# Kernel optimization log

Hardware: AMD Instinct MI355X
Metric: run time of the kernel (lower is better)

The kernel has to match this reference:

```python
import jax, jax.numpy as jnp
import numpy as np

DIM_S, DIM_A, DIM_C, H, T = 64, 8, 16, 256, 262144
LOG_STD_MIN, LOG_STD_MAX = -5.0, 2.0


def _linear_init(k, fin, fout):
    k1, k2 = jax.random.split(k)
    lim = 1.0 / np.sqrt(fin)
    W = jax.random.uniform(k1, (fin, fout), minval=-lim, maxval=lim, dtype=jnp.float32)
    b = jax.random.uniform(k2, (fout,), minval=-lim, maxval=lim, dtype=jnp.float32)
    return W, b


def setup_inputs() -> dict:
    key = jax.random.key(0)
    ks = jax.random.split(key, 8)
    pW1, pb1 = _linear_init(ks[0], DIM_S, H)
    pW2, pb2 = _linear_init(ks[1], H, H)
    pW3, pb3 = _linear_init(ks[2], H, DIM_C * DIM_A)
    oW1, ob1 = _linear_init(ks[3], DIM_S, H)
    oW2, ob2 = _linear_init(ks[4], H, H)
    oW3, ob3 = _linear_init(ks[5], H, (DIM_C + 1) * DIM_C)
    a_log_std = jnp.zeros((1, DIM_A), jnp.float32)
    s_array = jax.random.normal(ks[6], (T, DIM_S), jnp.float32)
    a_array = jax.random.normal(ks[7], (T, DIM_A), jnp.float32)
    return dict(s_array=s_array, a_array=a_array,
                pW1=pW1, pb1=pb1, pW2=pW2, pb2=pb2, pW3=pW3, pb3=pb3,
                oW1=oW1, ob1=ob1, oW2=oW2, ob2=ob2, oW3=oW3, ob3=ob3,
                a_log_std=a_log_std)


def _mlp(x, W1, b1, W2, b2, W3, b3):
    h = jax.nn.relu(x @ W1 + b1)
    h = jax.nn.relu(h @ W2 + b2)
    return h @ W3 + b3


def reference(s_array, a_array, pW1, pb1, pW2, pb2, pW3, pb3,
              oW1, ob1, oW2, ob2, oW3, ob3, a_log_std):
    Tn = s_array.shape[0]
    # --- log_prob_action with ct=None: per-option Gaussian log-density ---
    mean = _mlp(s_array, pW1, pb1, pW2, pb2, pW3, pb3).reshape(Tn, DIM_C, DIM_A)
    mean = jnp.clip(mean, -10.0, 10.0)
    logstd = LOG_STD_MIN + 0.5 * (LOG_STD_MAX - LOG_STD_MIN) * (jnp.tanh(a_log_std) + 1.0)  # (1, A), shared across options
    std = jnp.exp(logstd)
    at = a_array[:, None, :]                                   # (T, 1, A)
    lp = -0.5 * ((at - mean) / std) ** 2 - logstd - 0.5 * jnp.log(2.0 * jnp.pi)
    log_pis = lp.sum(-1)                                       # (T, C)
    # --- log_trans: normalized option-transition logits ---
    logits = _mlp(s_array, oW1, ob1, oW2, ob2, oW3, ob3).reshape(Tn, DIM_C + 1, DIM_C)
    log_trs_full = jax.nn.log_softmax(logits, axis=-1)
    log_tr0 = log_trs_full[0, -1]                              # (C,) initial dist from c_{-1}=dim_c
    log_trs = log_trs_full[1:, :-1]                            # (T-1, C, C)
    # --- forward recursion (alpha) via scan ---
    a0 = log_tr0 + log_pis[0]
    def fwd_step(carry, x):
        ltr, lpi = x
        a = jax.nn.logsumexp(carry[:, None] + ltr, axis=0) + lpi
        return a, a
    _, alphas = jax.lax.scan(fwd_step, a0, (log_trs, log_pis[1:]))
    log_alpha = jnp.concatenate([a0[None], alphas], axis=0)    # (T, C)
    # --- backward recursion (beta) via reverse scan ---
    bT = jnp.zeros((DIM_C,), jnp.float32)
    def bwd_step(carry, x):
        ltr, lpi = x
        b = jax.nn.logsumexp((carry + lpi)[None, :] + ltr, axis=-1)
        return b, b
    _, betas = jax.lax.scan(bwd_step, bT, (log_trs, log_pis[1:]), reverse=True)
    log_beta = jnp.concatenate([betas, bT[None]], axis=0)      # (T, C)
    entropy = -(log_trs * jnp.exp(log_trs)).sum(-1)            # (T-1, C)
    return (log_alpha, log_beta, log_trs, log_pis, entropy)
```

## Files before the change

### kernel.cpp

```cpp
#include <hip/hip_runtime.h>
#include <hip/hip_bf16.h>
#include <math.h>

#define T_N   262144
#define NSTEP (T_N - 1)
#define CS    256
#define NC    1024
#define NG    32

#define OFF_A   ((size_t)0)
#define OFF_B   ((size_t)4194304)
#define OFF_LTR ((size_t)8388608)
#define OFF_LPI ((size_t)75497216)
#define OFF_ENT ((size_t)79691520)

#define WS_TR0  ((size_t)0)
#define WS_M    ((size_t)64)
#define WS_LP   (WS_M  + (size_t)NC*256)
#define WS_LS   (WS_LP + (size_t)NC*256)
#define WS_GT   (WS_LS + (size_t)NC*256)
#define WS_GP   (WS_GT + (size_t)NG*256)
#define WS_GSU  (WS_GP + (size_t)NG*256)
#define WS_PREF (WS_GSU + (size_t)NG*256)
#define WS_SUF  (WS_PREF + (size_t)NC*256)
#define WS_WP   (WS_SUF  + (size_t)NC*256)

#define O_pW1h 0
#define O_pW1l 16384
#define O_pW2h 32768
#define O_pW2l 98304
#define O_pW3h 163840
#define O_pW3l 196608
#define O_oW1h 229376
#define O_oW1l 245760
#define O_oW2h 262144
#define O_oW2l 327680
#define O_oW3h 393216
#define O_oW3l 462848

#define NEGINF (-1e30f)

typedef unsigned short ushort_t;
typedef short s8v __attribute__((ext_vector_type(8)));
typedef float f4v __attribute__((ext_vector_type(4)));

__device__ __forceinline__ ushort_t f2bf_rn(float f) {
  __hip_bfloat16 h = __float2bfloat16(f);
  union { __hip_bfloat16 b; ushort_t u; } cv; cv.b = h; return cv.u;
}
__device__ __forceinline__ float us2f(ushort_t u) {
  return __uint_as_float(((unsigned)u) << 16);
}
__device__ __forceinline__ void split_bf(float x, ushort_t& h, ushort_t& lo) {
  unsigned u = __float_as_uint(x);
  h = (ushort_t)(u >> 16);
  lo = f2bf_rn(x - __uint_as_float(u & 0xffff0000u));
}

__global__ void k_pack(const float* __restrict__ W, int KN, int NT, int N,
                       ushort_t* __restrict__ dh, ushort_t* __restrict__ dl)
{
  int idx = blockIdx.x * 256 + threadIdx.x;
  if (idx >= KN) return;
  int j  = idx & 7;
  int l  = (idx >> 3) & 63;
  int t2 = idx >> 9;
  int nt = t2 % NT;
  int ks = t2 / NT;
  int k = ks * 32 + (l >> 4) * 8 + j;
  int n = nt * 16 + (l & 15);
  float x = W[(size_t)k * N + n];
  unsigned u = __float_as_uint(x);
  dh[idx] = (ushort_t)(u >> 16);
  dl[idx] = f2bf_rn(x - __uint_as_float(u & 0xffff0000u));
}


#define LDX 72
#define LDH 264

template<int KS, int NTC>
__device__ __forceinline__ void run_layer(const ushort_t* Ah, const ushort_t* Al, int lda,
    const ushort_t* __restrict__ Bh, const ushort_t* __restrict__ Bl, int ntt, int nt0,
    const float* __restrict__ bias, int lane, f4v (&acc)[2][NTC])
{
#pragma unroll
  for (int mt = 0; mt < 2; mt++)
#pragma unroll
    for (int nt = 0; nt < NTC; nt++) {
      float b = bias[(nt0 + nt) * 16 + (lane & 15)];
      acc[mt][nt] = (f4v){b, b, b, b};
    }
  for (int ks = 0; ks < KS; ks++) {
    s8v ah[2], al[2];
#pragma unroll
    for (int mt = 0; mt < 2; mt++) {
      const ushort_t* p = Ah + (size_t)(mt * 16 + (lane & 15)) * lda + ks * 32 + (lane >> 4) * 8;
      ah[mt] = *(const s8v*)p;
      const ushort_t* q = Al + (size_t)(mt * 16 + (lane & 15)) * lda + ks * 32 + (lane >> 4) * 8;
      al[mt] = *(const s8v*)q;
    }
#pragma unroll
    for (int nt = 0; nt < NTC; nt++) {
      size_t bo = ((size_t)(ks * ntt + nt0 + nt) * 64 + lane) * 8;
      s8v bh = *(const s8v*)(Bh + bo);
      s8v bl = *(const s8v*)(Bl + bo);
#pragma unroll
      for (int mt = 0; mt < 2; mt++) {
        acc[mt][nt] = __builtin_amdgcn_mfma_f32_16x16x32_bf16(ah[mt], bh, acc[mt][nt], 0, 0, 0);
        acc[mt][nt] = __builtin_amdgcn_mfma_f32_16x16x32_bf16(al[mt], bh, acc[mt][nt], 0, 0, 0);
        acc[mt][nt] = __builtin_amdgcn_mfma_f32_16x16x32_bf16(ah[mt], bl, acc[mt][nt], 0, 0, 0);
      }
    }
  }
}

__device__ __forceinline__ void store_act(f4v (&acc)[2][4], int nt0, int lane,
                                          ushort_t* Hh, ushort_t* Hl)
{
#pragma unroll
  for (int mt = 0; mt < 2; mt++)
#pragma unroll
    for (int nt = 0; nt < 4; nt++)
#pragma unroll
      for (int r = 0; r < 4; r++) {
        float v = fmaxf(acc[mt][nt][r], 0.f);
        ushort_t h, lo; split_bf(v, h, lo);
        int row = mt * 16 + (lane >> 4) * 4 + r;
        int n = (nt0 + nt) * 16 + (lane & 15);
        Hh[row * LDH + n] = h;
        Hl[row * LDH + n] = lo;
      }
}

__launch_bounds__(256, 3)
__global__ void k_mlp2(const float* __restrict__ s_array, const float* __restrict__ a_array,
                       const float* __restrict__ pb1, const float* __restrict__ pb2,
                       const float* __restrict__ pb3, const float* __restrict__ ob1,
                       const float* __restrict__ ob2, const float* __restrict__ ob3,
                       const float* __restrict__ oW3, const float* __restrict__ als,
                       const ushort_t* __restrict__ wp, float* out, float* ws)
{
  __shared__ ushort_t Xh[32 * LDX], Xl[32 * LDX];
  __shared__ ushort_t Hh[32 * LDH], Hl[32 * LDH];
  __shared__ float tr0s[16];
  const int tid = threadIdx.x;
  const int lane = tid & 63;
  const int w = tid >> 6;
  const size_t row0 = (size_t)blockIdx.x * 32;

  {
    const float4* src = (const float4*)(s_array + row0 * 64);
    for (int f = tid; f < 512; f += 256) {
      float4 v = src[f];
      int r = f >> 4, c = (f & 15) * 4;
      ushort_t h0, l0, h1, l1, h2, l2, h3, l3;
      split_bf(v.x, h0, l0); split_bf(v.y, h1, l1);
      split_bf(v.z, h2, l2); split_bf(v.w, h3, l3);
      ushort4 hh = make_ushort4(h0, h1, h2, h3);
      ushort4 ll = make_ushort4(l0, l1, l2, l3);
      *(ushort4*)&Xh[r * LDX + c] = hh;
      *(ushort4*)&Xl[r * LDX + c] = ll;
    }
  }
  __syncthreads();

  f4v acc[2][4];

  run_layer<2, 4>(Xh, Xl, LDX, wp + O_oW1h, wp + O_oW1l, 16, w * 4, ob1, lane, acc);
  store_act(acc, w * 4, lane, Hh, Hl);
  __syncthreads();
  run_layer<8, 4>(Hh, Hl, LDH, wp + O_oW2h, wp + O_oW2l, 16, w * 4, ob2, lane, acc);
  __syncthreads();
  store_act(acc, w * 4, lane, Hh, Hl);
  __syncthreads();
  run_layer<8, 4>(Hh, Hl, LDH, wp + O_oW3h, wp + O_oW3l, 17, w * 4, ob3, lane, acc);

#pragma unroll
  for (int mt = 0; mt < 2; mt++)
#pragma unroll
    for (int nt = 0; nt < 4; nt++) {
      int g = w * 4 + nt;
      int col = lane & 15;
#pragma unroll
      for (int r = 0; r < 4; r++) {
        size_t t = row0 + mt * 16 + (lane >> 4) * 4 + r;
        float x = acc[mt][nt][r];
        float m = x;
        m = fmaxf(m, __shfl_xor(m, 1, 64));
        m = fmaxf(m, __shfl_xor(m, 2, 64));
        m = fmaxf(m, __shfl_xor(m, 4, 64));
        m = fmaxf(m, __shfl_xor(m, 8, 64));
        float s = __expf(x - m);
        s += __shfl_xor(s, 1, 64);
        s += __shfl_xor(s, 2, 64);
        s += __shfl_xor(s, 4, 64);
        s += __shfl_xor(s, 8, 64);
        float L = m + __logf(s);
        float v = x - L;
        float e = -v * __expf(v);
        e += __shfl_xor(e, 1, 64);
        e += __shfl_xor(e, 2, 64);
        e += __shfl_xor(e, 4, 64);
        e += __shfl_xor(e, 8, 64);
        if (t >= 1) {
          out[OFF_LTR + (t - 1) * 256 + (size_t)g * 16 + col] = v;
          if (col == 0) out[OFF_ENT + (t - 1) * 16 + g] = e;
        }
      }
    }

  if (blockIdx.x == 0 && tid < 16) {
    float a = ob3[256 + tid];
    for (int k2 = 0; k2 < 256; k2++) {
      float hv = us2f(Hh[k2]) + us2f(Hl[k2]);
      a = fmaf(hv, oW3[(size_t)k2 * 272 + 256 + tid], a);
    }
    tr0s[tid] = a;
  }
  __syncthreads();
  if (blockIdx.x == 0 && tid == 0) {
    float m = NEGINF;
    for (int j = 0; j < 16; j++) m = fmaxf(m, tr0s[j]);
    float s = 0.f;
    for (int j = 0; j < 16; j++) s += __expf(tr0s[j] - m);
    float L = m + __logf(s);
    for (int j = 0; j < 16; j++) ws[WS_TR0 + j] = tr0s[j] - L;
  }

  run_layer<2, 4>(Xh, Xl, LDX, wp + O_pW1h, wp + O_pW1l, 16, w * 4, pb1, lane, acc);
  store_act(acc, w * 4, lane, Hh, Hl);
  __syncthreads();
  run_layer<8, 4>(Hh, Hl, LDH, wp + O_pW2h, wp + O_pW2l, 16, w * 4, pb2, lane, acc);
  __syncthreads();
  store_act(acc, w * 4, lane, Hh, Hl);
  __syncthreads();
  f4v pacc[2][2];
  run_layer<8, 2>(Hh, Hl, LDH, wp + O_pW3h, wp + O_pW3l, 8, w * 2, pb3, lane, pacc);

  float istd[8];
  float Kc = -8.0f * 0.91893853320467274f;
#pragma unroll
  for (int a = 0; a < 8; a++) {
    float l = -5.0f + 3.5f * (tanhf(als[a]) + 1.0f);
    istd[a] = __expf(-l);
    Kc -= l;
  }
  int aIdx = lane & 7;
#pragma unroll
  for (int mt = 0; mt < 2; mt++)
#pragma unroll
    for (int nt = 0; nt < 2; nt++) {
      int col = (w * 2 + nt) * 16 + (lane & 15);
      int c = col >> 3;
#pragma unroll
      for (int r = 0; r < 4; r++) {
        size_t t = row0 + mt * 16 + (lane >> 4) * 4 + r;
        float mean = fminf(10.f, fmaxf(-10.f, pacc[mt][nt][r]));
        float av = a_array[t * 8 + aIdx];
        float z = (av - mean) * istd[aIdx];
        float q = z * z;
        q += __shfl_xor(q, 1, 64);
        q += __shfl_xor(q, 2, 64);
        q += __shfl_xor(q, 4, 64);
        if ((lane & 7) == 0) out[OFF_LPI + t * 16 + c] = -0.5f * q + Kc;
      }
    }
}


#define LDA 20

__launch_bounds__(256, 4)
__global__ void k_compose(const float* __restrict__ out, float* __restrict__ ws)
{
  __shared__ float AsT[2][16 * LDA] __attribute__((aligned(16)));
  __shared__ float Mb[2][16 * 16] __attribute__((aligned(16)));
  __shared__ float Lsb[2][16];
  const int tid = threadIdx.x;
  const int i = tid >> 4, k = tid & 15;
  const int c = blockIdx.x;
  long long e0 = (long long)c * CS;
  long long e1 = e0 + CS; if (e1 > NSTEP) e1 = NSTEP;

  float a1, l1;
  {
    float a0 = out[OFF_LTR + (size_t)e0 * 256 + tid];
    AsT[0][k * LDA + i] = a0;
    if (tid < 16) Lsb[0][tid] = out[OFF_LPI + (size_t)(e0 + 1) * 16 + tid];
    Mb[0][tid] = (i == k) ? 0.f : NEGINF;
    a1 = out[OFF_LTR + (size_t)(e0 + 1) * 256 + tid];
    l1 = (tid < 16) ? out[OFF_LPI + (size_t)(e0 + 2) * 16 + tid] : 0.f;
  }
  __syncthreads();

  int cur = 0;
  float last = NEGINF;
  for (long long e = e0; e < e1; e++) {
    float a2 = out[OFF_LTR + (size_t)(e + 2) * 256 + tid];
    float l2 = (tid < 16) ? out[OFF_LPI + (size_t)(e + 3) * 16 + tid] : 0.f;

    float v[16];
    {
      const float4* M4 = (const float4*)&Mb[cur][i * 16];
      const float4* A4 = (const float4*)&AsT[cur][k * LDA];
#pragma unroll
      for (int t = 0; t < 4; t++) {
        float4 a = M4[t], b = A4[t];
        v[4 * t + 0] = a.x + b.x; v[4 * t + 1] = a.y + b.y;
        v[4 * t + 2] = a.z + b.z; v[4 * t + 3] = a.w + b.w;
      }
    }
    float m = NEGINF;
#pragma unroll
    for (int j = 0; j < 16; j++) m = fmaxf(m, v[j]);
    float s = 0.f;
#pragma unroll
    for (int j = 0; j < 16; j++) s += __expf(v[j] - m);
    last = m + __logf(s) + Lsb[cur][k];

    AsT[cur ^ 1][k * LDA + i] = a1;
    if (tid < 16) Lsb[cur ^ 1][tid] = l1;
    Mb[cur ^ 1][tid] = last;
    __syncthreads();
    a1 = a2; l1 = l2;
    cur ^= 1;
  }
  ws[WS_M + (size_t)c * 256 + tid] = last;
}


__launch_bounds__(256, 4)
__global__ void k_scan_mats(const float* __restrict__ src, float* __restrict__ preDst,
                            float* __restrict__ sufDst, float* __restrict__ totDst)
{
  __shared__ float Cur[16 * 17];
  const int tid = threadIdx.x, i = tid >> 4, k = tid & 15;
  const int g = blockIdx.x;
  const float* S = src + (size_t)g * 32 * 256;
  const float id = (i == k) ? 0.f : NEGINF;

  float rv[16], rn[16];
  Cur[i * 17 + k] = id;
#pragma unroll
  for (int j = 0; j < 16; j++) rv[j] = S[j * 16 + k];
  __syncthreads();
  for (int r = 0; r < 32; r++) {
    preDst[((size_t)g * 32 + r) * 256 + tid] = Cur[i * 17 + k];
    int rp = (r + 1 < 32) ? r + 1 : 31;
#pragma unroll
    for (int j = 0; j < 16; j++) rn[j] = S[(size_t)rp * 256 + j * 16 + k];
    float v[16]; float m = NEGINF;
#pragma unroll
    for (int j = 0; j < 16; j++) { v[j] = Cur[i * 17 + j] + rv[j]; m = fmaxf(m, v[j]); }
    float s = 0.f;
#pragma unroll
    for (int j = 0; j < 16; j++) s += __expf(v[j] - m);
    float res = m + __logf(s);
    __syncthreads();
    Cur[i * 17 + k] = res;
    __syncthreads();
#pragma unroll
    for (int j = 0; j < 16; j++) rv[j] = rn[j];
  }
  if (totDst) totDst[(size_t)g * 256 + tid] = Cur[i * 17 + k];
  __syncthreads();
  Cur[i * 17 + k] = id;
#pragma unroll
  for (int j = 0; j < 16; j++) rv[j] = S[(size_t)31 * 256 + i * 16 + j];
  __syncthreads();
  for (int r = 31; r >= 0; r--) {
    sufDst[((size_t)g * 32 + r) * 256 + tid] = Cur[i * 17 + k];
    int rp = (r > 0) ? r - 1 : 0;
#pragma unroll
    for (int j = 0; j < 16; j++) rn[j] = S[(size_t)rp * 256 + i * 16 + j];
    float v[16]; float m = NEGINF;
#pragma unroll
    for (int j = 0; j < 16; j++) { v[j] = rv[j] + Cur[j * 17 + k]; m = fmaxf(m, v[j]); }
    float s = 0.f;
#pragma unroll
    for (int j = 0; j < 16; j++) s += __expf(v[j] - m);
    float res = m + __logf(s);
    __syncthreads();
    Cur[i * 17 + k] = res;
    __syncthreads();
#pragma unroll
    for (int j = 0; j < 16; j++) rv[j] = rn[j];
  }
}


__launch_bounds__(256, 4)
__global__ void k_combine(float* ws)
{
  const int tid = threadIdx.x, i = tid >> 4, k = tid & 15;
  const int c = blockIdx.x, g = c >> 5;
  {
    const float* GP = ws + WS_GP + (size_t)g * 256;
    const float* LP = ws + WS_LP + (size_t)c * 256;
    float v[16]; float m = NEGINF;
#pragma unroll
    for (int j = 0; j < 16; j++) { v[j] = GP[i * 16 + j] + LP[j * 16 + k]; m = fmaxf(m, v[j]); }
    float s = 0.f;
#pragma unroll
    for (int j = 0; j < 16; j++) s += __expf(v[j] - m);
    ws[WS_PREF + (size_t)c * 256 + tid] = m + __logf(s);
  }
  {
    const float* LSu = ws + WS_LS + (size_t)c * 256;
    const float* GSu = ws + WS_GSU + (size_t)g * 256;
    float v[16]; float m = NEGINF;
#pragma unroll
    for (int j = 0; j < 16; j++) { v[j] = LSu[i * 16 + j] + GSu[j * 16 + k]; m = fmaxf(m, v[j]); }
    float s = 0.f;
#pragma unroll
    for (int j = 0; j < 16; j++) s += __expf(v[j] - m);
    ws[WS_SUF + (size_t)c * 256 + tid] = m + __logf(s);
  }
}


__device__ __forceinline__ void lse_combine(float& m, float& s, int mask)
{
  float m2 = __shfl_xor(m, mask, 64);
  float s2 = __shfl_xor(s, mask, 64);
  float M_ = fmaxf(m, m2);
  s = s * __expf(m - M_) + s2 * __expf(m2 - M_);
  m = M_;
}

__launch_bounds__(128, 4)
__global__ void k_replay(const float* __restrict__ ws, float* out)
{
  const int c = blockIdx.x;
  long long e0 = (long long)c * CS;
  long long e1 = e0 + CS; if (e1 > NSTEP) e1 = NSTEP;
  const int lane = threadIdx.x & 63;
  const int wv = threadIdx.x >> 6;
  const int x = lane & 15;
  const int q = lane >> 4;

  if (wv == 0) {
    if (c == 0 && lane < 16)
      out[OFF_A + lane] = ws[WS_TR0 + lane] + out[OFF_LPI + lane];
    const float* P = ws + WS_PREF + (size_t)c * 256;
    float v4[4]; float m = NEGINF;
#pragma unroll
    for (int t2 = 0; t2 < 4; t2++) {
      int i2 = 4 * q + t2;
      float a0i = ws[WS_TR0 + i2] + out[OFF_LPI + i2];
      float vv = a0i + P[i2 * 16 + x];
      v4[t2] = vv; m = fmaxf(m, vv);
    }
    float s = 0.f;
#pragma unroll
    for (int t2 = 0; t2 < 4; t2++) s += __expf(v4[t2] - m);
    lse_combine(m, s, 16); lse_combine(m, s, 32);
    float cv = m + __logf(s);
    float vq[4];
#pragma unroll
    for (int t2 = 0; t2 < 4; t2++) vq[t2] = __shfl(cv, q * 4 + t2, 64);

    float ta0[4], ta1[4], la0, la1;
#pragma unroll
    for (int t2 = 0; t2 < 4; t2++)
      ta0[t2] = out[OFF_LTR + (size_t)e0 * 256 + (size_t)(4 * q + t2) * 16 + x];
    la0 = out[OFF_LPI + (size_t)(e0 + 1) * 16 + x];
#pragma unroll
    for (int t2 = 0; t2 < 4; t2++)
      ta1[t2] = out[OFF_LTR + (size_t)(e0 + 1) * 256 + (size_t)(4 * q + t2) * 16 + x];
    la1 = out[OFF_LPI + (size_t)(e0 + 2) * 16 + x];

    for (long long e = e0; e < e1; e++) {
      float tn[4], ln;
#pragma unroll
      for (int t2 = 0; t2 < 4; t2++)
        tn[t2] = out[OFF_LTR + (size_t)(e + 2) * 256 + (size_t)(4 * q + t2) * 16 + x];
      ln = out[OFF_LPI + (size_t)(e + 3) * 16 + x];

      long long t = e + 1;
      float w4[4]; float m2 = NEGINF;
#pragma unroll
      for (int t2 = 0; t2 < 4; t2++) {
        float vvv = vq[t2] + ta0[t2];
        w4[t2] = vvv; m2 = fmaxf(m2, vvv);
      }
      float s2 = 0.f;
#pragma unroll
      for (int t2 = 0; t2 < 4; t2++) s2 += __expf(w4[t2] - m2);
      lse_combine(m2, s2, 16); lse_combine(m2, s2, 32);
      float nv = m2 + __logf(s2) + la0;
      if (lane < 16) out[OFF_A + (size_t)t * 16 + x] = nv;
#pragma unroll
      for (int t2 = 0; t2 < 4; t2++) vq[t2] = __shfl(nv, q * 4 + t2, 64);
#pragma unroll
      for (int t2 = 0; t2 < 4; t2++) { ta0[t2] = ta1[t2]; ta1[t2] = tn[t2]; }
      la0 = la1; la1 = ln;
    }
  } else {
    if (c == NC - 1 && lane < 16) out[OFF_B + (size_t)(T_N - 1) * 16 + lane] = 0.f;
    const float* Sf = ws + WS_SUF + (size_t)c * 256;
    float v4[4]; float m = NEGINF;
#pragma unroll
    for (int t2 = 0; t2 < 4; t2++) {
      float vv = Sf[x * 16 + 4 * q + t2];
      v4[t2] = vv; m = fmaxf(m, vv);
    }
    float s = 0.f;
#pragma unroll
    for (int t2 = 0; t2 < 4; t2++) s += __expf(v4[t2] - m);
    lse_combine(m, s, 16); lse_combine(m, s, 32);
    float u = m + __logf(s);
    float uq[4];
#pragma unroll
    for (int t2 = 0; t2 < 4; t2++) uq[t2] = __shfl(u, q * 4 + t2, 64);

    float tb0[4], tb1[4], lb0[4], lb1[4];
    {
      long long eA = e1 - 1, eB = e1 - 2;
      float4 f = *(const float4*)&out[(long long)OFF_LTR + eA * 256 + x * 16 + 4 * q];
      tb0[0] = f.x; tb0[1] = f.y; tb0[2] = f.z; tb0[3] = f.w;
      float4 g2 = *(const float4*)&out[(long long)OFF_LPI + (eA + 1) * 16 + 4 * q];
      lb0[0] = g2.x; lb0[1] = g2.y; lb0[2] = g2.z; lb0[3] = g2.w;
      float4 f2 = *(const float4*)&out[(long long)OFF_LTR + eB * 256 + x * 16 + 4 * q];
      tb1[0] = f2.x; tb1[1] = f2.y; tb1[2] = f2.z; tb1[3] = f2.w;
      float4 g3 = *(const float4*)&out[(long long)OFF_LPI + (eB + 1) * 16 + 4 * q];
      lb1[0] = g3.x; lb1[1] = g3.y; lb1[2] = g3.z; lb1[3] = g3.w;
    }

    for (long long e = e1 - 1; e >= e0; e--) {
      float tn[4], ln[4];
      {
        long long ep = e - 2;
        float4 f = *(const float4*)&out[(long long)OFF_LTR + ep * 256 + x * 16 + 4 * q];
        tn[0] = f.x; tn[1] = f.y; tn[2] = f.z; tn[3] = f.w;
        float4 g2 = *(const float4*)&out[(long long)OFF_LPI + (ep + 1) * 16 + 4 * q];
        ln[0] = g2.x; ln[1] = g2.y; ln[2] = g2.z; ln[3] = g2.w;
      }
      float w4[4]; float m2 = NEGINF;
#pragma unroll
      for (int t2 = 0; t2 < 4; t2++) {
        float vvv = tb0[t2] + lb0[t2] + uq[t2];
        w4[t2] = vvv; m2 = fmaxf(m2, vvv);
      }
      float s2 = 0.f;
#pragma unroll
      for (int t2 = 0; t2 < 4; t2++) s2 += __expf(w4[t2] - m2);
      lse_combine(m2, s2, 16); lse_combine(m2, s2, 32);
      float b = m2 + __logf(s2);
      if (lane < 16) out[OFF_B + (size_t)e * 16 + x] = b;
#pragma unroll
      for (int t2 = 0; t2 < 4; t2++) uq[t2] = __shfl(b, q * 4 + t2, 64);
#pragma unroll
      for (int t2 = 0; t2 < 4; t2++) {
        tb0[t2] = tb1[t2]; tb1[t2] = tn[t2];
        lb0[t2] = lb1[t2]; lb1[t2] = ln[t2];
      }
    }
  }
}


extern "C" void kernel_launch(void* const* d_in, const int* in_sizes, int n_in,
                              void* d_out, int out_size, void* d_ws, size_t ws_size,
                              hipStream_t stream)
{
  const float* s_array = (const float*)d_in[0];
  const float* a_array = (const float*)d_in[1];
  const float* pW1 = (const float*)d_in[2];
  const float* pb1 = (const float*)d_in[3];
  const float* pW2 = (const float*)d_in[4];
  const float* pb2 = (const float*)d_in[5];
  const float* pW3 = (const float*)d_in[6];
  const float* pb3 = (const float*)d_in[7];
  const float* oW1 = (const float*)d_in[8];
  const float* ob1 = (const float*)d_in[9];
  const float* oW2 = (const float*)d_in[10];
  const float* ob2 = (const float*)d_in[11];
  const float* oW3 = (const float*)d_in[12];
  const float* ob3 = (const float*)d_in[13];
  const float* als = (const float*)d_in[14];
  float* out = (float*)d_out;
  float* ws  = (float*)d_ws;
  ushort_t* wp = (ushort_t*)(ws + WS_WP);

  hipLaunchKernelGGL(k_pack, dim3(64),  dim3(256), 0, stream, pW1, 16384, 16, 256, wp + O_pW1h, wp + O_pW1l);
  hipLaunchKernelGGL(k_pack, dim3(256), dim3(256), 0, stream, pW2, 65536, 16, 256, wp + O_pW2h, wp + O_pW2l);
  hipLaunchKernelGGL(k_pack, dim3(128), dim3(256), 0, stream, pW3, 32768,  8, 128, wp + O_pW3h, wp + O_pW3l);
  hipLaunchKernelGGL(k_pack, dim3(64),  dim3(256), 0, stream, oW1, 16384, 16, 256, wp + O_oW1h, wp + O_oW1l);
  hipLaunchKernelGGL(k_pack, dim3(256), dim3(256), 0, stream, oW2, 65536, 16, 256, wp + O_oW2h, wp + O_oW2l);
  hipLaunchKernelGGL(k_pack, dim3(272), dim3(256), 0, stream, oW3, 69632, 17, 272, wp + O_oW3h, wp + O_oW3l);

  hipLaunchKernelGGL(k_mlp2, dim3(T_N / 32), dim3(256), 0, stream,
                     s_array, a_array, pb1, pb2, pb3, ob1, ob2, ob3, oW3, als,
                     (const ushort_t*)wp, out, ws);
  hipLaunchKernelGGL(k_compose, dim3(NC), dim3(256), 0, stream, out, ws);
  hipLaunchKernelGGL(k_scan_mats, dim3(NG), dim3(256), 0, stream,
                     ws + WS_M, ws + WS_LP, ws + WS_LS, ws + WS_GT);
  hipLaunchKernelGGL(k_scan_mats, dim3(1), dim3(256), 0, stream,
                     ws + WS_GT, ws + WS_GP, ws + WS_GSU, (float*)nullptr);
  hipLaunchKernelGGL(k_combine, dim3(NC), dim3(256), 0, stream, ws);
  hipLaunchKernelGGL(k_replay, dim3(NC), dim3(128), 0, stream, ws, out);
}
```

Measured before the change: 1.546 ms.

## Use wave-per-chunk shuffle-based log-semiring composition with finer chunking

Rewrites the chunk composition and hierarchical scan kernels so that one wavefront, rather than a whole block, handles each chunk. Each lane computes four outputs and the new row is broadcast with shuffles, which replaces the block-wide barrier on every step. The scan runs its forward and backward directions in separate waves, and the log-sum-exp uses a tree reduction. It also adds a finer chunking configuration (4096 chunks of 64 steps) that is selected when the workspace is large enough. The trade-off is more intermediate matrices to write, plus a fallback path to the old chunk sizes when the workspace is smaller.

```diff
diff --git a/kernel.cpp b/kernel.cpp
--- a/kernel.cpp
+++ b/kernel.cpp
@@ -4,9 +4,6 @@
 
 #define T_N   262144
 #define NSTEP (T_N - 1)
-#define CS    256
-#define NC    1024
-#define NG    32
 
 #define OFF_A   ((size_t)0)
 #define OFF_B   ((size_t)4194304)
@@ -15,15 +12,6 @@
 #define OFF_ENT ((size_t)79691520)
 
 #define WS_TR0  ((size_t)0)
-#define WS_M    ((size_t)64)
-#define WS_LP   (WS_M  + (size_t)NC*256)
-#define WS_LS   (WS_LP + (size_t)NC*256)
-#define WS_GT   (WS_LS + (size_t)NC*256)
-#define WS_GP   (WS_GT + (size_t)NG*256)
-#define WS_GSU  (WS_GP + (size_t)NG*256)
-#define WS_PREF (WS_GSU + (size_t)NG*256)
-#define WS_SUF  (WS_PREF + (size_t)NC*256)
-#define WS_WP   (WS_SUF  + (size_t)NC*256)
 
 #define O_pW1h 0
 #define O_pW1l 16384
@@ -43,6 +31,23 @@
 typedef unsigned short ushort_t;
 typedef short s8v __attribute__((ext_vector_type(8)));
 typedef float f4v __attribute__((ext_vector_type(4)));
+
+struct CfgBig   { static constexpr int NC2 = 4096, CS2 = 64,  NG2 = 128; };
+struct CfgSmall { static constexpr int NC2 = 1024, CS2 = 256, NG2 = 32;  };
+
+template<class C> struct WSO {
+  static constexpr size_t TR0  = 0;
+  static constexpr size_t M    = 64;
+  static constexpr size_t LP   = M    + (size_t)C::NC2 * 256;
+  static constexpr size_t LS   = LP   + (size_t)C::NC2 * 256;
+  static constexpr size_t GT   = LS   + (size_t)C::NC2 * 256;
+  static constexpr size_t GP   = GT   + (size_t)C::NG2 * 256;
+  static constexpr size_t GSU  = GP   + (size_t)C::NG2 * 256;
+  static constexpr size_t PREF = GSU  + (size_t)C::NG2 * 256;
+  static constexpr size_t SUF  = PREF + (size_t)C::NC2 * 256;
+  static constexpr size_t WP   = SUF  + (size_t)C::NC2 * 256;
+  static constexpr size_t TOTAL_BYTES = (WP + 266240 + 64) * 4;
+};
 
 __device__ __forceinline__ ushort_t f2bf_rn(float f) {
   __hip_bfloat16 h = __float2bfloat16(f);
@@ -268,157 +273,229 @@
     }
 }
 
-
-#define LDA 20
-
-__launch_bounds__(256, 4)
-__global__ void k_compose(const float* __restrict__ out, float* __restrict__ ws)
-{
-  __shared__ float AsT[2][16 * LDA] __attribute__((aligned(16)));
-  __shared__ float Mb[2][16 * 16] __attribute__((aligned(16)));
-  __shared__ float Lsb[2][16];
-  const int tid = threadIdx.x;
-  const int i = tid >> 4, k = tid & 15;
-  const int c = blockIdx.x;
-  long long e0 = (long long)c * CS;
-  long long e1 = e0 + CS; if (e1 > NSTEP) e1 = NSTEP;
-
-  float a1, l1;
-  {
-    float a0 = out[OFF_LTR + (size_t)e0 * 256 + tid];
-    AsT[0][k * LDA + i] = a0;
-    if (tid < 16) Lsb[0][tid] = out[OFF_LPI + (size_t)(e0 + 1) * 16 + tid];
-    Mb[0][tid] = (i == k) ? 0.f : NEGINF;
-    a1 = out[OFF_LTR + (size_t)(e0 + 1) * 256 + tid];
-    l1 = (tid < 16) ? out[OFF_LPI + (size_t)(e0 + 2) * 16 + tid] : 0.f;
-  }
-  __syncthreads();
+__device__ __forceinline__ float lse16v(const float* v)
+{
+  float m01 = fmaxf(v[0], v[1]),   m23 = fmaxf(v[2], v[3]);
+  float m45 = fmaxf(v[4], v[5]),   m67 = fmaxf(v[6], v[7]);
+  float m89 = fmaxf(v[8], v[9]),   mab = fmaxf(v[10], v[11]);
+  float mcd = fmaxf(v[12], v[13]), mef = fmaxf(v[14], v[15]);
+  float ma = fmaxf(fmaxf(m01, m23), fmaxf(m45, m67));
+  float mb = fmaxf(fmaxf(m89, mab), fmaxf(mcd, mef));
+  float m = fmaxf(ma, mb);
+  float s0 = __expf(v[0] - m) + __expf(v[1] - m);
+  float s1 = __expf(v[2] - m) + __expf(v[3] - m);
+  float s2 = __expf(v[4] - m) + __expf(v[5] - m);
+  float s3 = __expf(v[6] - m) + __expf(v[7] - m);
+  float s4 = __expf(v[8] - m) + __expf(v[9] - m);
+  float s5 = __expf(v[10] - m) + __expf(v[11] - m);
+  float s6 = __expf(v[12] - m) + __expf(v[13] - m);
+  float s7 = __expf(v[14] - m) + __expf(v[15] - m);
+  float s = ((s0 + s1) + (s2 + s3)) + ((s4 + s5) + (s6 + s7));
+  return m + __logf(s);
+}
+
+__device__ __forceinline__ void step_right(float (&Mrow)[16], const float* __restrict__ A,
+                                           int lane, float4 ls, float (&own)[4])
+{
+  const int kq = lane & 3;
+  float v0[16], v1[16], v2[16], v3[16];
+#pragma unroll
+  for (int j = 0; j < 16; j++) {
+    float4 a = *(const float4*)(A + j * 16 + kq * 4);
+    v0[j] = Mrow[j] + a.x;
+    v1[j] = Mrow[j] + a.y;
+    v2[j] = Mrow[j] + a.z;
+    v3[j] = Mrow[j] + a.w;
+  }
+  float nv0 = lse16v(v0) + ls.x;
+  float nv1 = lse16v(v1) + ls.y;
+  float nv2 = lse16v(v2) + ls.z;
+  float nv3 = lse16v(v3) + ls.w;
+  own[0] = nv0; own[1] = nv1; own[2] = nv2; own[3] = nv3;
+  const int base = lane & 60;
+#pragma unroll
+  for (int q2 = 0; q2 < 4; q2++) {
+    Mrow[q2 * 4 + 0] = __shfl(nv0, base | q2, 64);
+    Mrow[q2 * 4 + 1] = __shfl(nv1, base | q2, 64);
+    Mrow[q2 * 4 + 2] = __shfl(nv2, base | q2, 64);
+    Mrow[q2 * 4 + 3] = __shfl(nv3, base | q2, 64);
+  }
+}
+
+__device__ __forceinline__ void step_left(float (&Scol)[16], const float* __restrict__ A,
+                                          int lane, float (&own)[4])
+{
+  const int iq = lane & 3;
+  float v0[16], v1[16], v2[16], v3[16];
+#pragma unroll
+  for (int jj = 0; jj < 4; jj++) {
+    float4 a0 = *(const float4*)(A + (iq * 4 + 0) * 16 + jj * 4);
+    float4 a1 = *(const float4*)(A + (iq * 4 + 1) * 16 + jj * 4);
+    float4 a2 = *(const float4*)(A + (iq * 4 + 2) * 16 + jj * 4);
+    float4 a3 = *(const float4*)(A + (iq * 4 + 3) * 16 + jj * 4);
+    v0[jj*4+0] = a0.x + Scol[jj*4+0]; v0[jj*4+1] = a0.y + Scol[jj*4+1];
+    v0[jj*4+2] = a0.z + Scol[jj*4+2]; v0[jj*4+3] = a0.w + Scol[jj*4+3];
+    v1[jj*4+0] = a1.x + Scol[jj*4+0]; v1[jj*4+1] = a1.y + Scol[jj*4+1];
+    v1[jj*4+2] = a1.z + Scol[jj*4+2]; v1[jj*4+3] = a1.w + Scol[jj*4+3];
+    v2[jj*4+0] = a2.x + Scol[jj*4+0]; v2[jj*4+1] = a2.y + Scol[jj*4+1];
+    v2[jj*4+2] = a2.z + Scol[jj*4+2]; v2[jj*4+3] = a2.w + Scol[jj*4+3];
+    v3[jj*4+0] = a3.x + Scol[jj*4+0]; v3[jj*4+1] = a3.y + Scol[jj*4+1];
+    v3[jj*4+2] = a3.z + Scol[jj*4+2]; v3[jj*4+3] = a3.w + Scol[jj*4+3];
+  }
+  float nv0 = lse16v(v0);
+  float nv1 = lse16v(v1);
+  float nv2 = lse16v(v2);
+  float nv3 = lse16v(v3);
+  own[0] = nv0; own[1] = nv1; own[2] = nv2; own[3] = nv3;
+  const int base = lane & 60;
+#pragma unroll
+  for (int q2 = 0; q2 < 4; q2++) {
+    Scol[q2 * 4 + 0] = __shfl(nv0, base | q2, 64);
+    Scol[q2 * 4 + 1] = __shfl(nv1, base | q2, 64);
+    Scol[q2 * 4 + 2] = __shfl(nv2, base | q2, 64);
+    Scol[q2 * 4 + 3] = __shfl(nv3, base | q2, 64);
+  }
+}
+
+template<class C>
+__launch_bounds__(256, 3)
+__global__ void k_composeW(const float* __restrict__ out, float* __restrict__ ws)
+{
+  __shared__ float Abuf[4][2][256] __attribute__((aligned(16)));
+  const int tid = threadIdx.x, lane = tid & 63, w = tid >> 6;
+  const int kq = lane & 3, i = lane >> 2;
+  const long long c = (long long)blockIdx.x * 4 + w;
+  long long e0 = c * C::CS2;
+  long long e1 = e0 + C::CS2; if (e1 > NSTEP) e1 = NSTEP;
+
+  float Mrow[16], own[4];
+#pragma unroll
+  for (int j = 0; j < 16; j++) Mrow[j] = (j == i) ? 0.f : NEGINF;
+#pragma unroll
+  for (int kk = 0; kk < 4; kk++) own[kk] = (kq * 4 + kk == i) ? 0.f : NEGINF;
+
+  const float* LT = out + OFF_LTR;
+  const float* LPp = out + OFF_LPI;
+  float4 gB = *(const float4*)(LT + e0 * 256 + lane * 4);
+  float4 gC = *(const float4*)(LT + (e0 + 1) * 256 + lane * 4);
+  float4 lA = *(const float4*)(LPp + (e0 + 1) * 16 + kq * 4);
+  float4 lB = *(const float4*)(LPp + (e0 + 2) * 16 + kq * 4);
+  float4 lC = *(const float4*)(LPp + (e0 + 3) * 16 + kq * 4);
+  *(float4*)(&Abuf[w][0][lane * 4]) = gB;
+  gB = gC;
+  gC = *(const float4*)(LT + (e0 + 2) * 256 + lane * 4);
 
   int cur = 0;
-  float last = NEGINF;
   for (long long e = e0; e < e1; e++) {
-    float a2 = out[OFF_LTR + (size_t)(e + 2) * 256 + tid];
-    float l2 = (tid < 16) ? out[OFF_LPI + (size_t)(e + 3) * 16 + tid] : 0.f;
-
-    float v[16];
-    {
-      const float4* M4 = (const float4*)&Mb[cur][i * 16];
-      const float4* A4 = (const float4*)&AsT[cur][k * LDA];
-#pragma unroll
-      for (int t = 0; t < 4; t++) {
-        float4 a = M4[t], b = A4[t];
-        v[4 * t + 0] = a.x + b.x; v[4 * t + 1] = a.y + b.y;
-        v[4 * t + 2] = a.z + b.z; v[4 * t + 3] = a.w + b.w;
-      }
-    }
-    float m = NEGINF;
-#pragma unroll
-    for (int j = 0; j < 16; j++) m = fmaxf(m, v[j]);
-    float s = 0.f;
-#pragma unroll
-    for (int j = 0; j < 16; j++) s += __expf(v[j] - m);
-    last = m + __logf(s) + Lsb[cur][k];
-
-    AsT[cur ^ 1][k * LDA + i] = a1;
-    if (tid < 16) Lsb[cur ^ 1][tid] = l1;
-    Mb[cur ^ 1][tid] = last;
-    __syncthreads();
-    a1 = a2; l1 = l2;
+    float4 gN = *(const float4*)(LT + (e + 3) * 256 + lane * 4);
+    float4 lN = *(const float4*)(LPp + (e + 4) * 16 + kq * 4);
+    *(float4*)(&Abuf[w][cur ^ 1][lane * 4]) = gB;
+    step_right(Mrow, &Abuf[w][cur][0], lane, lA, own);
+    gB = gC; gC = gN; lA = lB; lB = lC; lC = lN;
     cur ^= 1;
   }
-  ws[WS_M + (size_t)c * 256 + tid] = last;
-}
-
-
-__launch_bounds__(256, 4)
-__global__ void k_scan_mats(const float* __restrict__ src, float* __restrict__ preDst,
-                            float* __restrict__ sufDst, float* __restrict__ totDst)
-{
-  __shared__ float Cur[16 * 17];
-  const int tid = threadIdx.x, i = tid >> 4, k = tid & 15;
-  const int g = blockIdx.x;
-  const float* S = src + (size_t)g * 32 * 256;
-  const float id = (i == k) ? 0.f : NEGINF;
-
-  float rv[16], rn[16];
-  Cur[i * 17 + k] = id;
-#pragma unroll
-  for (int j = 0; j < 16; j++) rv[j] = S[j * 16 + k];
-  __syncthreads();
-  for (int r = 0; r < 32; r++) {
-    preDst[((size_t)g * 32 + r) * 256 + tid] = Cur[i * 17 + k];
-    int rp = (r + 1 < 32) ? r + 1 : 31;
-#pragma unroll
-    for (int j = 0; j < 16; j++) rn[j] = S[(size_t)rp * 256 + j * 16 + k];
-    float v[16]; float m = NEGINF;
-#pragma unroll
-    for (int j = 0; j < 16; j++) { v[j] = Cur[i * 17 + j] + rv[j]; m = fmaxf(m, v[j]); }
-    float s = 0.f;
-#pragma unroll
-    for (int j = 0; j < 16; j++) s += __expf(v[j] - m);
-    float res = m + __logf(s);
-    __syncthreads();
-    Cur[i * 17 + k] = res;
-    __syncthreads();
-#pragma unroll
-    for (int j = 0; j < 16; j++) rv[j] = rn[j];
-  }
-  if (totDst) totDst[(size_t)g * 256 + tid] = Cur[i * 17 + k];
-  __syncthreads();
-  Cur[i * 17 + k] = id;
-#pragma unroll
-  for (int j = 0; j < 16; j++) rv[j] = S[(size_t)31 * 256 + i * 16 + j];
-  __syncthreads();
-  for (int r = 31; r >= 0; r--) {
-    sufDst[((size_t)g * 32 + r) * 256 + tid] = Cur[i * 17 + k];
-    int rp = (r > 0) ? r - 1 : 0;
-#pragma unroll
-    for (int j = 0; j < 16; j++) rn[j] = S[(size_t)rp * 256 + i * 16 + j];
-    float v[16]; float m = NEGINF;
-#pragma unroll
-    for (int j = 0; j < 16; j++) { v[j] = rv[j] + Cur[j * 17 + k]; m = fmaxf(m, v[j]); }
-    float s = 0.f;
-#pragma unroll
-    for (int j = 0; j < 16; j++) s += __expf(v[j] - m);
-    float res = m + __logf(s);
-    __syncthreads();
-    Cur[i * 17 + k] = res;
-    __syncthreads();
-#pragma unroll
-    for (int j = 0; j < 16; j++) rv[j] = rn[j];
-  }
-}
-
-
+  float4 st; st.x = own[0]; st.y = own[1]; st.z = own[2]; st.w = own[3];
+  *(float4*)(ws + WSO<C>::M + (size_t)c * 256 + i * 16 + kq * 4) = st;
+}
+
+template<class C, int LEN>
+__launch_bounds__(256, 2)
+__global__ void k_scanW(const float* __restrict__ src, float* __restrict__ preDst,
+                        float* __restrict__ sufDst, float* __restrict__ totDst, int ngroups)
+{
+  __shared__ float Abuf[4][2][256] __attribute__((aligned(16)));
+  const int tid = threadIdx.x, lane = tid & 63, w = tid >> 6;
+  const int grp = blockIdx.x * 2 + (w >> 1);
+  const int dir = w & 1;
+  if (grp >= ngroups) return;
+  const float* S = src + (size_t)grp * LEN * 256;
+
+  if (dir == 0) {
+    const int kq = lane & 3, i = lane >> 2;
+    float Mrow[16], own[4];
+#pragma unroll
+    for (int j = 0; j < 16; j++) Mrow[j] = (j == i) ? 0.f : NEGINF;
+#pragma unroll
+    for (int kk = 0; kk < 4; kk++) own[kk] = (kq * 4 + kk == i) ? 0.f : NEGINF;
+    const float4 zero4 = make_float4(0.f, 0.f, 0.f, 0.f);
+
+    float4 gB = *(const float4*)(S + lane * 4);
+    float4 gC = *(const float4*)(S + 256 + lane * 4);
+    *(float4*)(&Abuf[w][0][lane * 4]) = gB;
+    gB = gC;
+    gC = *(const float4*)(S + 2 * 256 + lane * 4);
+    int cur = 0;
+    for (int r = 0; r < LEN; r++) {
+      int rn = (r + 3 < LEN) ? r + 3 : LEN - 1;
+      float4 gN = *(const float4*)(S + (size_t)rn * 256 + lane * 4);
+      *(float4*)(&Abuf[w][cur ^ 1][lane * 4]) = gB;
+      float4 st; st.x = own[0]; st.y = own[1]; st.z = own[2]; st.w = own[3];
+      *(float4*)(preDst + ((size_t)grp * LEN + r) * 256 + i * 16 + kq * 4) = st;
+      step_right(Mrow, &Abuf[w][cur][0], lane, zero4, own);
+      gB = gC; gC = gN; cur ^= 1;
+    }
+    if (totDst) {
+      float4 st; st.x = own[0]; st.y = own[1]; st.z = own[2]; st.w = own[3];
+      *(float4*)(totDst + (size_t)grp * 256 + i * 16 + kq * 4) = st;
+    }
+  } else {
+    const int iq = lane & 3, k = lane >> 2;
+    float Scol[16], own[4];
+#pragma unroll
+    for (int j = 0; j < 16; j++) Scol[j] = (j == k) ? 0.f : NEGINF;
+#pragma unroll
+    for (int t = 0; t < 4; t++) own[t] = (iq * 4 + t == k) ? 0.f : NEGINF;
+
+    float4 gB = *(const float4*)(S + (size_t)(LEN - 1) * 256 + lane * 4);
+    float4 gC = *(const float4*)(S + (size_t)(LEN - 2) * 256 + lane * 4);
+    *(float4*)(&Abuf[w][0][lane * 4]) = gB;
+    gB = gC;
+    gC = *(const float4*)(S + (size_t)(LEN - 3) * 256 + lane * 4);
+    int cur = 0;
+    for (int r = LEN - 1; r >= 0; r--) {
+      int rn = (r - 3 >= 0) ? r - 3 : 0;
+      float4 gN = *(const float4*)(S + (size_t)rn * 256 + lane * 4);
+      *(float4*)(&Abuf[w][cur ^ 1][lane * 4]) = gB;
+      size_t base = ((size_t)grp * LEN + r) * 256;
+      sufDst[base + (iq * 4 + 0) * 16 + k] = own[0];
+      sufDst[base + (iq * 4 + 1) * 16 + k] = own[1];
+      sufDst[base + (iq * 4 + 2) * 16 + k] = own[2];
+      sufDst[base + (iq * 4 + 3) * 16 + k] = own[3];
+      step_left(Scol, &Abuf[w][cur][0], lane, own);
+      gB = gC; gC = gN; cur ^= 1;
+    }
+  }
+}
+
+template<class C>
 __launch_bounds__(256, 4)
 __global__ void k_combine(float* ws)
 {
   const int tid = threadIdx.x, i = tid >> 4, k = tid & 15;
   const int c = blockIdx.x, g = c >> 5;
   {
-    const float* GP = ws + WS_GP + (size_t)g * 256;
-    const float* LP = ws + WS_LP + (size_t)c * 256;
+    const float* GP = ws + WSO<C>::GP + (size_t)g * 256;
+    const float* LP = ws + WSO<C>::LP + (size_t)c * 256;
     float v[16]; float m = NEGINF;
 #pragma unroll
     for (int j = 0; j < 16; j++) { v[j] = GP[i * 16 + j] + LP[j * 16 + k]; m = fmaxf(m, v[j]); }
     float s = 0.f;
 #pragma unroll
     for (int j = 0; j < 16; j++) s += __expf(v[j] - m);
-    ws[WS_PREF + (size_t)c * 256 + tid] = m + __logf(s);
+    ws[WSO<C>::PREF + (size_t)c * 256 + tid] = m + __logf(s);
   }
   {
-    const float* LSu = ws + WS_LS + (size_t)c * 256;
-    const float* GSu = ws + WS_GSU + (size_t)g * 256;
+    const float* LSu = ws + WSO<C>::LS + (size_t)c * 256;
+    const float* GSu = ws + WSO<C>::GSU + (size_t)g * 256;
     float v[16]; float m = NEGINF;
 #pragma unroll
     for (int j = 0; j < 16; j++) { v[j] = LSu[i * 16 + j] + GSu[j * 16 + k]; m = fmaxf(m, v[j]); }
     float s = 0.f;
 #pragma unroll
     for (int j = 0; j < 16; j++) s += __expf(v[j] - m);
-    ws[WS_SUF + (size_t)c * 256 + tid] = m + __logf(s);
-  }
-}
-
+    ws[WSO<C>::SUF + (size_t)c * 256 + tid] = m + __logf(s);
+  }
+}
 
 __device__ __forceinline__ void lse_combine(float& m, float& s, int mask)
 {
@@ -429,12 +506,13 @@
   m = M_;
 }
 
+template<class C>
 __launch_bounds__(128, 4)
 __global__ void k_replay(const float* __restrict__ ws, float* out)
 {
   const int c = blockIdx.x;
-  long long e0 = (long long)c * CS;
-  long long e1 = e0 + CS; if (e1 > NSTEP) e1 = NSTEP;
+  long long e0 = (long long)c * C::CS2;
+  long long e1 = e0 + C::CS2; if (e1 > NSTEP) e1 = NSTEP;
   const int lane = threadIdx.x & 63;
   const int wv = threadIdx.x >> 6;
   const int x = lane & 15;
@@ -442,13 +520,13 @@
 
   if (wv == 0) {
     if (c == 0 && lane < 16)
-      out[OFF_A + lane] = ws[WS_TR0 + lane] + out[OFF_LPI + lane];
-    const float* P = ws + WS_PREF + (size_t)c * 256;
+      out[OFF_A + lane] = ws[WSO<C>::TR0 + lane] + out[OFF_LPI + lane];
+    const float* P = ws + WSO<C>::PREF + (size_t)c * 256;
     float v4[4]; float m = NEGINF;
 #pragma unroll
     for (int t2 = 0; t2 < 4; t2++) {
       int i2 = 4 * q + t2;
-      float a0i = ws[WS_TR0 + i2] + out[OFF_LPI + i2];
+      float a0i = ws[WSO<C>::TR0 + i2] + out[OFF_LPI + i2];
       float vv = a0i + P[i2 * 16 + x];
       v4[t2] = vv; m = fmaxf(m, vv);
     }
@@ -498,8 +576,8 @@
       la0 = la1; la1 = ln;
     }
   } else {
-    if (c == NC - 1 && lane < 16) out[OFF_B + (size_t)(T_N - 1) * 16 + lane] = 0.f;
-    const float* Sf = ws + WS_SUF + (size_t)c * 256;
+    if (c == C::NC2 - 1 && lane < 16) out[OFF_B + (size_t)(T_N - 1) * 16 + lane] = 0.f;
+    const float* Sf = ws + WSO<C>::SUF + (size_t)c * 256;
     float v4[4]; float m = NEGINF;
 #pragma unroll
     for (int t2 = 0; t2 < 4; t2++) {
@@ -560,6 +638,35 @@
   }
 }
 
+
+template<class C>
+static void launch_all(const float* s_array, const float* a_array,
+                       const float* pW1, const float* pb1, const float* pW2, const float* pb2,
+                       const float* pW3, const float* pb3, const float* oW1, const float* ob1,
+                       const float* oW2, const float* ob2, const float* oW3, const float* ob3,
+                       const float* als, float* out, float* ws, hipStream_t stream)
+{
+  ushort_t* wp = (ushort_t*)(ws + WSO<C>::WP);
+
+  hipLaunchKernelGGL(k_pack, dim3(64),  dim3(256), 0, stream, pW1, 16384, 16, 256, wp + O_pW1h, wp + O_pW1l);
+  hipLaunchKernelGGL(k_pack, dim3(256), dim3(256), 0, stream, pW2, 65536, 16, 256, wp + O_pW2h, wp + O_pW2l);
+  hipLaunchKernelGGL(k_pack, dim3(128), dim3(256), 0, stream, pW3, 32768,  8, 128, wp + O_pW3h, wp + O_pW3l);
+  hipLaunchKernelGGL(k_pack, dim3(64),  dim3(256), 0, stream, oW1, 16384, 16, 256, wp + O_oW1h, wp + O_oW1l);
+  hipLaunchKernelGGL(k_pack, dim3(256), dim3(256), 0, stream, oW2, 65536, 16, 256, wp + O_oW2h, wp + O_oW2l);
+  hipLaunchKernelGGL(k_pack, dim3(272), dim3(256), 0, stream, oW3, 69632, 17, 272, wp + O_oW3h, wp + O_oW3l);
+
+  hipLaunchKernelGGL(k_mlp2, dim3(T_N / 32), dim3(256), 0, stream,
+                     s_array, a_array, pb1, pb2, pb3, ob1, ob2, ob3, oW3, als,
+                     (const ushort_t*)wp, out, ws);
+
+  hipLaunchKernelGGL((k_composeW<C>), dim3(C::NC2 / 4), dim3(256), 0, stream, out, ws);
+  hipLaunchKernelGGL((k_scanW<C, 32>), dim3(C::NG2 / 2), dim3(256), 0, stream,
+                     ws + WSO<C>::M, ws + WSO<C>::LP, ws + WSO<C>::LS, ws + WSO<C>::GT, C::NG2);
+  hipLaunchKernelGGL((k_scanW<C, C::NG2>), dim3(1), dim3(128), 0, stream,
+                     ws + WSO<C>::GT, ws + WSO<C>::GP, ws + WSO<C>::GSU, (float*)nullptr, 1);
+  hipLaunchKernelGGL((k_combine<C>), dim3(C::NC2), dim3(256), 0, stream, ws);
+  hipLaunchKernelGGL((k_replay<C>), dim3(C::NC2), dim3(128), 0, stream, ws, out);
+}
 
 extern "C" void kernel_launch(void* const* d_in, const int* in_sizes, int n_in,
                               void* d_out, int out_size, void* d_ws, size_t ws_size,
@@ -582,23 +689,12 @@
   const float* als = (const float*)d_in[14];
   float* out = (float*)d_out;
   float* ws  = (float*)d_ws;
-  ushort_t* wp = (ushort_t*)(ws + WS_WP);
-
-  hipLaunchKernelGGL(k_pack, dim3(64),  dim3(256), 0, stream, pW1, 16384, 16, 256, wp + O_pW1h, wp + O_pW1l);
-  hipLaunchKernelGGL(k_pack, dim3(256), dim3(256), 0, stream, pW2, 65536, 16, 256, wp + O_pW2h, wp + O_pW2l);
-  hipLaunchKernelGGL(k_pack, dim3(128), dim3(256), 0, stream, pW3, 32768,  8, 128, wp + O_pW3h, wp + O_pW3l);
-  hipLaunchKernelGGL(k_pack, dim3(64),  dim3(256), 0, stream, oW1, 16384, 16, 256, wp + O_oW1h, wp + O_oW1l);
-  hipLaunchKernelGGL(k_pack, dim3(256), dim3(256), 0, stream, oW2, 65536, 16, 256, wp + O_oW2h, wp + O_oW2l);
-  hipLaunchKernelGGL(k_pack, dim3(272), dim3(256), 0, stream, oW3, 69632, 17, 272, wp + O_oW3h, wp + O_oW3l);
-
-  hipLaunchKernelGGL(k_mlp2, dim3(T_N / 32), dim3(256), 0, stream,
-                     s_array, a_array, pb1, pb2, pb3, ob1, ob2, ob3, oW3, als,
-                     (const ushort_t*)wp, out, ws);
-  hipLaunchKernelGGL(k_compose, dim3(NC), dim3(256), 0, stream, out, ws);
-  hipLaunchKernelGGL(k_scan_mats, dim3(NG), dim3(256), 0, stream,
-                     ws + WS_M, ws + WS_LP, ws + WS_LS, ws + WS_GT);
-  hipLaunchKernelGGL(k_scan_mats, dim3(1), dim3(256), 0, stream,
-                     ws + WS_GT, ws + WS_GP, ws + WS_GSU, (float*)nullptr);
-  hipLaunchKernelGGL(k_combine, dim3(NC), dim3(256), 0, stream, ws);
-  hipLaunchKernelGGL(k_replay, dim3(NC), dim3(128), 0, stream, ws, out);
-}
+
+  if (ws_size >= WSO<CfgBig>::TOTAL_BYTES) {
+    launch_all<CfgBig>(s_array, a_array, pW1, pb1, pW2, pb2, pW3, pb3,
+                       oW1, ob1, oW2, ob2, oW3, ob3, als, out, ws, stream);
+  } else {
+    launch_all<CfgSmall>(s_array, a_array, pW1, pb1, pW2, pb2, pW3, pb3,
+                         oW1, ob1, oW2, ob2, oW3, ob3, als, out, ws, stream);
+  }
+}
```

Result: faster. 1.515 ms (-2.0%).
